# Optimization experiments

Hardware: AMD Instinct MI355X
Metric: run time of the kernel (lower is better)

Reference implementation:

```python
import jax, jax.numpy as jnp
import numpy as np

N_NODES = 30000
N_EDGES = 240000
N_GRAPHS = 300
IN_CH = 5


def _bn(x, p):
    # inference batchnorm; p = stack([gamma, beta, running_mean, running_var]), shape (4, C)
    g, b, m, v = p
    return g * (x - m) * jax.lax.rsqrt(v + 1e-5) + b


def _gatv2(x, src, dst, wl, bl, wr, br, att, bias, heads, outc, concat):
    # PyG GATv2Conv: e_ij = att . leaky_relu(lin_l(x_j) + lin_r(x_i)), softmax over edges into i,
    # out_i = sum_j alpha_ij * lin_l(x_j)
    n = x.shape[0]
    xl = (x @ wl + bl).reshape(n, heads, outc)  # source-side transform
    xr = (x @ wr + br).reshape(n, heads, outc)  # target-side transform
    e = jax.nn.leaky_relu(xl[src] + xr[dst], 0.2)          # [E, H, C]
    logit = jnp.einsum('ehc,hc->eh', e, att)               # [E, H]
    lmax = jax.ops.segment_max(logit, dst, num_segments=n)
    lmax = jnp.where(jnp.isfinite(lmax), lmax, 0.0)        # empty segments -> 0
    ex = jnp.exp(logit - lmax[dst])
    den = jax.ops.segment_sum(ex, dst, num_segments=n)
    alpha = ex / (den[dst] + 1e-16)                        # PyG softmax eps
    out = jax.ops.segment_sum(xl[src] * alpha[..., None], dst, num_segments=n)
    out = out.reshape(n, heads * outc) if concat else out.mean(axis=1)
    return out + bias


def _forward(x, edge_index, batch, w_in, b_in, bn_in,
             g1_wl, g1_bl, g1_wr, g1_br, g1_att, g1_bias, bn1,
             g2_wl, g2_bl, g2_wr, g2_br, g2_att, g2_bias, bn2,
             g3_wl, g3_bl, g3_wr, g3_br, g3_att, g3_bias, bn3,
             c_w1, c_b1, c_bn, c_w2, c_b2, c_w3, c_b3):
    n = x.shape[0]
    loops = jnp.arange(n)
    src = jnp.concatenate([edge_index[0], loops])  # add_self_loops=True
    dst = jnp.concatenate([edge_index[1], loops])
    h = jax.nn.relu(_bn(x @ w_in + b_in, bn_in))
    h = jax.nn.elu(_bn(_gatv2(h, src, dst, g1_wl, g1_bl, g1_wr, g1_br, g1_att, g1_bias, 4, 64, True), bn1))
    h = jax.nn.elu(_bn(_gatv2(h, src, dst, g2_wl, g2_bl, g2_wr, g2_br, g2_att, g2_bias, 4, 64, True), bn2))
    h = jax.nn.elu(_bn(_gatv2(h, src, dst, g3_wl, g3_bl, g3_wr, g3_br, g3_att, g3_bias, 1, 128, False), bn3))
    cnt = jax.ops.segment_sum(jnp.ones((n,), h.dtype), batch, num_segments=N_GRAPHS)
    mean = jax.ops.segment_sum(h, batch, num_segments=N_GRAPHS) / jnp.maximum(cnt, 1.0)[:, None]
    mx = jax.ops.segment_max(h, batch, num_segments=N_GRAPHS)
    mx = jnp.where(jnp.isfinite(mx), mx, 0.0)
    g = jnp.concatenate([mean, mx], axis=1)                # (B, 256)
    z = jax.nn.relu(_bn(g @ c_w1 + c_b1, c_bn))
    z = jax.nn.relu(z @ c_w2 + c_b2)
    return jax.nn.log_softmax(z @ c_w3 + c_b3, axis=-1)    # (B, 2)


def setup_inputs() -> dict:
    base = jax.random.key(0)
    k = lambda i: jax.random.fold_in(base, i)
    def lin(i, fi, fo):
        return jax.random.normal(k(i), (fi, fo), jnp.float32) / np.sqrt(np.float32(fi))
    def vec(i, c):
        return jax.random.normal(k(i), (c,), jnp.float32) * 0.05
    def bn(i, c):
        g = jax.random.uniform(k(i), (c,), jnp.float32) + 0.5
        b = jax.random.normal(jax.random.fold_in(k(i), 1), (c,), jnp.float32) * 0.1
        return jnp.stack([g, b, jnp.zeros((c,), jnp.float32), jnp.ones((c,), jnp.float32)])
    def att(i, h, c):
        return jax.random.normal(k(i), (h, c), jnp.float32) / np.sqrt(np.float32(c))
    return dict(
        x=jax.random.normal(k(0), (N_NODES, IN_CH), jnp.float32),
        edge_index=jax.random.randint(k(1), (2, N_EDGES), 0, N_NODES),
        batch=jnp.sort(jax.random.randint(k(2), (N_NODES,), 0, N_GRAPHS)),
        w_in=lin(3, IN_CH, 64), b_in=vec(4, 64), bn_in=bn(5, 64),
        g1_wl=lin(6, 64, 256), g1_bl=vec(7, 256), g1_wr=lin(8, 64, 256), g1_br=vec(9, 256),
        g1_att=att(10, 4, 64), g1_bias=vec(11, 256), bn1=bn(12, 256),
        g2_wl=lin(13, 256, 256), g2_bl=vec(14, 256), g2_wr=lin(15, 256, 256), g2_br=vec(16, 256),
        g2_att=att(17, 4, 64), g2_bias=vec(18, 256), bn2=bn(19, 256),
        g3_wl=lin(20, 256, 128), g3_bl=vec(21, 128), g3_wr=lin(22, 256, 128), g3_br=vec(23, 128),
        g3_att=att(24, 1, 128), g3_bias=vec(25, 128), bn3=bn(26, 128),
        c_w1=lin(27, 256, 128), c_b1=vec(28, 128), c_bn=bn(29, 128),
        c_w2=lin(30, 128, 64), c_b2=vec(31, 64),
        c_w3=lin(32, 64, 2), c_b3=vec(33, 2),
    )


def reference(x, edge_index, batch, w_in, b_in, bn_in,
              g1_wl, g1_bl, g1_wr, g1_br, g1_att, g1_bias, bn1,
              g2_wl, g2_bl, g2_wr, g2_br, g2_att, g2_bias, bn2,
              g3_wl, g3_bl, g3_wr, g3_br, g3_att, g3_bias, bn3,
              c_w1, c_b1, c_bn, c_w2, c_b2, c_w3, c_b3):
    return _forward(x, edge_index, batch, w_in, b_in, bn_in,
                    g1_wl, g1_bl, g1_wr, g1_br, g1_att, g1_bias, bn1,
                    g2_wl, g2_bl, g2_wr, g2_br, g2_att, g2_bias, bn2,
                    g3_wl, g3_bl, g3_wr, g3_br, g3_att, g3_bias, bn3,
                    c_w1, c_b1, c_bn, c_w2, c_b2, c_w3, c_b3)
```

## Files before the change

### kernel.cpp

```cpp
#include <hip/hip_runtime.h>
#include <math.h>

#define N_NODES  30000
#define N_EDGES  240000
#define E_TOT    270000
#define N_GRAPHS 300
#define NCH      118

typedef _Float16 half8 __attribute__((ext_vector_type(8)));
typedef _Float16 half4 __attribute__((ext_vector_type(4)));
typedef _Float16 half2v __attribute__((ext_vector_type(2)));
typedef float float4v __attribute__((ext_vector_type(4)));

static inline int cdiv(int a, int b) { return (a + b - 1) / b; }

__device__ inline void wp_dev(const float* __restrict__ W, _Float16* __restrict__ Wt,
                              int K, int CO, int gtid, int T) {
    int tot = K * CO;
    for (int i = gtid; i < tot; i += T) {
        int k = i / CO, c = i - k * CO;
        Wt[(size_t)c * K + k] = (_Float16)W[i];
    }
}

__global__ void hist_wprep_input(const int* __restrict__ ei, int* __restrict__ deg,
                                 const float* __restrict__ x, const float* __restrict__ w_in,
                                 const float* __restrict__ b_in, const float* __restrict__ bn_in,
                                 _Float16* __restrict__ a16,
                                 const float* __restrict__ w1l, const float* __restrict__ w1r,
                                 const float* __restrict__ w2l, const float* __restrict__ w2r,
                                 const float* __restrict__ w3l, const float* __restrict__ w3r,
                                 _Float16* __restrict__ t1l, _Float16* __restrict__ t1r,
                                 _Float16* __restrict__ t2l, _Float16* __restrict__ t2r,
                                 _Float16* __restrict__ t3l, _Float16* __restrict__ t3r) {
    int gtid = blockIdx.x * blockDim.x + threadIdx.x;
    int T = gridDim.x * blockDim.x;
    for (int e = gtid; e < E_TOT; e += T) {
        int d = (e < N_EDGES) ? ei[N_EDGES + e] : e - N_EDGES;
        atomicAdd(&deg[d], 1);
    }
    wp_dev(w1l, t1l, 64, 256, gtid, T);
    wp_dev(w1r, t1r, 64, 256, gtid, T);
    wp_dev(w2l, t2l, 256, 256, gtid, T);
    wp_dev(w2r, t2r, 256, 256, gtid, T);
    wp_dev(w3l, t3l, 256, 128, gtid, T);
    wp_dev(w3r, t3r, 256, 128, gtid, T);

    int lane = threadIdx.x & 63;
    int wv = blockIdx.x * (blockDim.x >> 6) + (threadIdx.x >> 6);
    int NW = gridDim.x * (blockDim.x >> 6);
    float g = bn_in[lane], be = bn_in[64 + lane];
    float m = bn_in[128 + lane], va = bn_in[192 + lane];
    float rs = rsqrtf(va + 1e-5f);
    float wcol[5];
#pragma unroll
    for (int ci = 0; ci < 5; ++ci) wcol[ci] = w_in[ci * 64 + lane];
    float bb = b_in[lane];
    for (int n = wv; n < N_NODES; n += NW) {
        float xv = (lane < 5) ? x[n * 5 + lane] : 0.f;
        float acc = bb;
#pragma unroll
        for (int ci = 0; ci < 5; ++ci)
            acc = fmaf(__shfl(xv, ci, 64), wcol[ci], acc);
        acc = g * (acc - m) * rs + be;
        a16[(size_t)n * 64 + lane] = (_Float16)fmaxf(acc, 0.f);
    }
}

__global__ __launch_bounds__(256)
void scan_all(const int* __restrict__ deg, const int* __restrict__ batch,
              int* __restrict__ row_start, int* __restrict__ gstart) {
    __shared__ int red[256];
    __shared__ int s[256];
    const int b = blockIdx.x, t = threadIdx.x;
    int pre = 0;
    for (int i = t; i < b * 256; i += 256) pre += deg[i];
    red[t] = pre;
    __syncthreads();
    for (int off = 128; off; off >>= 1) {
        if (t < off) red[t] += red[t + off];
        __syncthreads();
    }
    int base = red[0];
    int gid = b * 256 + t;
    int v = (gid < N_NODES) ? deg[gid] : 0;
    s[t] = v;
    __syncthreads();
    for (int off = 1; off < 256; off <<= 1) {
        int u = (t >= off) ? s[t - off] : 0;
        __syncthreads();
        s[t] += u;
        __syncthreads();
    }
    if (gid < N_NODES) row_start[gid] = base + s[t] - v;
    if (b == 0 && t == 0) row_start[N_NODES] = E_TOT;
    if (b == 0) {
        for (int g = t; g <= N_GRAPHS; g += 256) {
            int lo = 0, hi = N_NODES;
            while (lo < hi) {
                int mid = (lo + hi) >> 1;
                if (batch[mid] < g) lo = mid + 1;
                else                hi = mid;
            }
            gstart[g] = lo;
        }
    }
}

template<int K, int COUT, int SCAT>
__global__ __launch_bounds__(256, 3)
void gemm_mfma(const _Float16* __restrict__ A,
               const _Float16* __restrict__ Wtl, const float* __restrict__ bl,
               const _Float16* __restrict__ Wtr, const float* __restrict__ br,
               _Float16* __restrict__ outl, _Float16* __restrict__ outr,
               const int* __restrict__ ei, const int* __restrict__ row_start,
               int* __restrict__ cnt, int* __restrict__ esrc, int N) {
    constexpr int BM = 128, BN = 128, BK = 64;
    constexpr int LDK = BK + 8;
    constexpr int CSL = COUT / BN > 0 ? COUT / BN : 1;
    if (SCAT && blockIdx.y == 2 * CSL) {
        int gtid = blockIdx.x * blockDim.x + threadIdx.x;
        int T = gridDim.x * blockDim.x;
        for (int e = gtid; e < E_TOT; e += T) {
            int s, d;
            if (e < N_EDGES) { s = ei[e]; d = ei[N_EDGES + e]; }
            else             { s = e - N_EDGES; d = s; }
            int slot = row_start[d] + atomicAdd(&cnt[d], 1);
            esrc[slot] = s;
        }
        return;
    }
    __shared__ _Float16 As[BM][LDK];
    __shared__ _Float16 Bs[BN][LDK];
    const int tid  = threadIdx.x;
    const int wave = tid >> 6;
    const int lane = tid & 63;
    const int l15  = lane & 15;
    const int lq   = lane >> 4;
    const int n0   = blockIdx.x * BM;
    const int sel  = blockIdx.y / CSL;
    const int col0 = (blockIdx.y % CSL) * BN;
    const _Float16* Wt = sel ? Wtr : Wtl;
    const float* bias  = sel ? br : bl;
    _Float16* out      = sel ? outr : outl;

    float4v acc[2][8];
#pragma unroll
    for (int mi = 0; mi < 2; ++mi)
#pragma unroll
        for (int nt = 0; nt < 8; ++nt)
#pragma unroll
            for (int r = 0; r < 4; ++r) acc[mi][nt][r] = 0.f;

    for (int kt = 0; kt < K; kt += BK) {
#pragma unroll
        for (int p = 0; p < 4; ++p) {
            int idx = p * 256 + tid;
            int row = idx >> 3;
            int ch  = (idx & 7) * 8;
            int gn  = n0 + row;
            half8 v = {};
            if (gn < N) v = *(const half8*)(A + (size_t)gn * K + kt + ch);
            *(half8*)(&As[row][ch]) = v;
        }
#pragma unroll
        for (int p = 0; p < 4; ++p) {
            int idx = p * 256 + tid;
            int row = idx >> 3;
            int ch  = (idx & 7) * 8;
            half8 v = *(const half8*)(Wt + (size_t)(col0 + row) * K + kt + ch);
            *(half8*)(&Bs[row][ch]) = v;
        }
        __syncthreads();
#pragma unroll
        for (int kk = 0; kk < BK; kk += 32) {
            half8 af0 = *(const half8*)(&As[wave * 32 + l15][kk + lq * 8]);
            half8 af1 = *(const half8*)(&As[wave * 32 + 16 + l15][kk + lq * 8]);
#pragma unroll
            for (int nt = 0; nt < 8; ++nt) {
                half8 bf = *(const half8*)(&Bs[nt * 16 + l15][kk + lq * 8]);
                acc[0][nt] = __builtin_amdgcn_mfma_f32_16x16x32_f16(af0, bf, acc[0][nt], 0, 0, 0);
                acc[1][nt] = __builtin_amdgcn_mfma_f32_16x16x32_f16(af1, bf, acc[1][nt], 0, 0, 0);
            }
        }
        __syncthreads();
    }
#pragma unroll
    for (int mi = 0; mi < 2; ++mi)
#pragma unroll
        for (int nt = 0; nt < 8; ++nt) {
            int col = col0 + nt * 16 + l15;
            float bv = bias[col];
#pragma unroll
            for (int r = 0; r < 4; ++r) {
                int row = n0 + wave * 32 + mi * 16 + lq * 4 + r;
                if (row < N)
                    out[(size_t)row * COUT + col] = (_Float16)(acc[mi][nt][r] + bv);
            }
        }
}

template<typename TOUT>
__global__ __launch_bounds__(256)
void gat_gather4(const _Float16* __restrict__ xl, const _Float16* __restrict__ xr,
                 const int* __restrict__ row_start, const int* __restrict__ esrc,
                 const float* __restrict__ att, const float* __restrict__ gbias,
                 const float* __restrict__ bnp, TOUT* __restrict__ out) {
    constexpr int HC = 256, PER = 4, GROUP = 16;
    int node = (blockIdx.x * blockDim.x + threadIdx.x) >> 6;
    int lane = threadIdx.x & 63;
    if (node >= N_NODES) return;
    const int base = lane * PER;

    float rr[PER], av[PER], acc[PER];
    {
        half4 rv = *(const half4*)(xr + (size_t)node * HC + base);
#pragma unroll
        for (int k = 0; k < PER; ++k) rr[k] = (float)rv[k];
        *(float4*)av = *(const float4*)(att + base);
    }
#pragma unroll
    for (int k = 0; k < PER; ++k) acc[k] = 0.f;

    float l = 0.f;
    const int j0 = row_start[node], j1 = row_start[node + 1];
    for (int jc = j0; jc < j1; jc += 64) {
        int nedge = min(64, j1 - jc);
        int ev = (jc + lane < j1) ? esrc[jc + lane] : 0;
        for (int jj = 0; jj < nedge; jj += 4) {
            int s[4];
            bool val[4];
#pragma unroll
            for (int u = 0; u < 4; ++u) {
                int idx = jj + u;
                val[u] = idx < nedge;
                s[u] = __shfl(ev, val[u] ? idx : jj, 64);
            }
            float xs[4][PER];
#pragma unroll
            for (int u = 0; u < 4; ++u) {
                half4 xv = *(const half4*)(xl + (size_t)s[u] * HC + base);
#pragma unroll
                for (int k = 0; k < PER; ++k) xs[u][k] = (float)xv[k];
            }
            float pz[4];
#pragma unroll
            for (int u = 0; u < 4; ++u) {
                float pp = 0.f;
#pragma unroll
                for (int k = 0; k < PER; ++k) {
                    float v = xs[u][k] + rr[k];
                    v = (v > 0.f) ? v : 0.2f * v;
                    pp = fmaf(v, av[k], pp);
                }
                pz[u] = pp;
            }
#pragma unroll
            for (int off = GROUP / 2; off; off >>= 1) {
#pragma unroll
                for (int u = 0; u < 4; ++u) pz[u] += __shfl_xor(pz[u], off, 64);
            }
            float w[4];
#pragma unroll
            for (int u = 0; u < 4; ++u) w[u] = val[u] ? __expf(pz[u]) : 0.f;
            l += (w[0] + w[1]) + (w[2] + w[3]);
#pragma unroll
            for (int k = 0; k < PER; ++k)
                acc[k] += fmaf(w[0], xs[0][k],
                          fmaf(w[1], xs[1][k],
                          fmaf(w[2], xs[2][k], w[3] * xs[3][k])));
        }
    }
    float inv = 1.f / (l + 1e-16f);
    float o[PER];
#pragma unroll
    for (int k = 0; k < PER; ++k) {
        float v = fmaf(acc[k], inv, gbias[base + k]);
        float g  = bnp[base + k], be = bnp[HC + base + k];
        float mm = bnp[2 * HC + base + k], va = bnp[3 * HC + base + k];
        v = g * (v - mm) * rsqrtf(va + 1e-5f) + be;
        o[k] = (v > 0.f) ? v : (__expf(v) - 1.f);
    }
    half4 ov;
#pragma unroll
    for (int k = 0; k < PER; ++k) ov[k] = (_Float16)o[k];
    *(half4*)((_Float16*)out + (size_t)node * HC + base) = ov;
}

__global__ __launch_bounds__(256)
void gat_gather1(const _Float16* __restrict__ xl, const _Float16* __restrict__ xr,
                 const int* __restrict__ row_start, const int* __restrict__ esrc,
                 const float* __restrict__ att, const float* __restrict__ gbias,
                 const float* __restrict__ bnp, float* __restrict__ out) {
    constexpr int HC = 128, PER = 4;
    int node = (blockIdx.x * blockDim.x + threadIdx.x) >> 6;
    int lane = threadIdx.x & 63;
    if (node >= N_NODES) return;
    const int half = lane >> 5;
    const int base = (lane & 31) * PER;

    float rr[PER], av[PER], acc[PER];
    {
        half4 rv = *(const half4*)(xr + (size_t)node * HC + base);
#pragma unroll
        for (int k = 0; k < PER; ++k) rr[k] = (float)rv[k];
        *(float4*)av = *(const float4*)(att + base);
    }
#pragma unroll
    for (int k = 0; k < PER; ++k) acc[k] = 0.f;

    float l = 0.f;
    const int j0 = row_start[node], j1 = row_start[node + 1];
    for (int jc = j0; jc < j1; jc += 64) {
        int nedge = min(64, j1 - jc);
        int ev = (jc + lane < j1) ? esrc[jc + lane] : 0;
        for (int jj = 0; jj < nedge; jj += 8) {
            int s[4];
            bool val[4];
#pragma unroll
            for (int u = 0; u < 4; ++u) {
                int idx = jj + 2 * u + half;
                val[u] = idx < nedge;
                s[u] = __shfl(ev, val[u] ? idx : jj, 64);
            }
            float xs[4][PER];
#pragma unroll
            for (int u = 0; u < 4; ++u) {
                half4 xv = *(const half4*)(xl + (size_t)s[u] * HC + base);
#pragma unroll
                for (int k = 0; k < PER; ++k) xs[u][k] = (float)xv[k];
            }
            float pz[4];
#pragma unroll
            for (int u = 0; u < 4; ++u) {
                float pp = 0.f;
#pragma unroll
                for (int k = 0; k < PER; ++k) {
                    float v = xs[u][k] + rr[k];
                    v = (v > 0.f) ? v : 0.2f * v;
                    pp = fmaf(v, av[k], pp);
                }
                pz[u] = pp;
            }
#pragma unroll
            for (int off = 16; off; off >>= 1) {
#pragma unroll
                for (int u = 0; u < 4; ++u) pz[u] += __shfl_xor(pz[u], off, 64);
            }
            float w[4];
#pragma unroll
            for (int u = 0; u < 4; ++u) w[u] = val[u] ? __expf(pz[u]) : 0.f;
            l += (w[0] + w[1]) + (w[2] + w[3]);
#pragma unroll
            for (int k = 0; k < PER; ++k)
                acc[k] += fmaf(w[0], xs[0][k],
                          fmaf(w[1], xs[1][k],
                          fmaf(w[2], xs[2][k], w[3] * xs[3][k])));
        }
    }
    l += __shfl_xor(l, 32, 64);
#pragma unroll
    for (int k = 0; k < PER; ++k) acc[k] += __shfl_xor(acc[k], 32, 64);

    if (half == 0) {
        float inv = 1.f / (l + 1e-16f);
        float o[PER];
#pragma unroll
        for (int k = 0; k < PER; ++k) {
            float v = fmaf(acc[k], inv, gbias[base + k]);
            float g  = bnp[base + k], be = bnp[HC + base + k];
            float mm = bnp[2 * HC + base + k], va = bnp[3 * HC + base + k];
            v = g * (v - mm) * rsqrtf(va + 1e-5f) + be;
            o[k] = (v > 0.f) ? v : (__expf(v) - 1.f);
        }
        *(float4*)(out + (size_t)node * HC + base) = *(float4*)o;
    }
}

__global__ void pool_cls(const float* __restrict__ h, const int* __restrict__ gstart,
                         const float* __restrict__ w1, const float* __restrict__ b1,
                         const float* __restrict__ bnp,
                         const float* __restrict__ w2, const float* __restrict__ b2,
                         const float* __restrict__ w3, const float* __restrict__ b3,
                         float* __restrict__ out) {
    __shared__ float sg[256];
    __shared__ float sz1[128];
    __shared__ float sz2[64];
    __shared__ float sz3[2];
    int g = blockIdx.x, t = threadIdx.x;
    int a = gstart[g], b = gstart[g + 1];
    float sum = 0.f, mx = -INFINITY;
    for (int i = a; i < b; ++i) {
        float v = h[(size_t)i * 128 + t];
        sum += v;
        mx = fmaxf(mx, v);
    }
    sg[t]       = sum / fmaxf((float)(b - a), 1.f);
    sg[128 + t] = (b > a) ? mx : 0.f;
    __syncthreads();
    float acc = b1[t];
    for (int i = 0; i < 256; ++i) acc += sg[i] * w1[i * 128 + t];
    float ga = bnp[t], be = bnp[128 + t], m = bnp[256 + t], va = bnp[384 + t];
    acc = ga * (acc - m) * rsqrtf(va + 1e-5f) + be;
    sz1[t] = fmaxf(acc, 0.f);
    __syncthreads();
    if (t < 64) {
        float a2 = b2[t];
        for (int i = 0; i < 128; ++i) a2 += sz1[i] * w2[i * 64 + t];
        sz2[t] = fmaxf(a2, 0.f);
    }
    __syncthreads();
    if (t < 2) {
        float a3 = b3[t];
        for (int i = 0; i < 64; ++i) a3 += sz2[i] * w3[i * 2 + t];
        sz3[t] = a3;
    }
    __syncthreads();
    if (t < 2) {
        float mm = fmaxf(sz3[0], sz3[1]);
        float lse = mm + logf(expf(sz3[0] - mm) + expf(sz3[1] - mm));
        out[g * 2 + t] = sz3[t] - lse;
    }
}

extern "C" void kernel_launch(void* const* d_in, const int* in_sizes, int n_in,
                              void* d_out, int out_size, void* d_ws, size_t ws_size,
                              hipStream_t stream) {
    const float* x       = (const float*)d_in[0];
    const int*   ei      = (const int*)d_in[1];
    const int*   batch   = (const int*)d_in[2];
    const float* w_in    = (const float*)d_in[3];
    const float* b_in    = (const float*)d_in[4];
    const float* bn_in   = (const float*)d_in[5];
    const float* g1_wl   = (const float*)d_in[6];
    const float* g1_bl   = (const float*)d_in[7];
    const float* g1_wr   = (const float*)d_in[8];
    const float* g1_br   = (const float*)d_in[9];
    const float* g1_att  = (const float*)d_in[10];
    const float* g1_bias = (const float*)d_in[11];
    const float* bn1     = (const float*)d_in[12];
    const float* g2_wl   = (const float*)d_in[13];
    const float* g2_bl   = (const float*)d_in[14];
    const float* g2_wr   = (const float*)d_in[15];
    const float* g2_br   = (const float*)d_in[16];
    const float* g2_att  = (const float*)d_in[17];
    const float* g2_bias = (const float*)d_in[18];
    const float* bn2     = (const float*)d_in[19];
    const float* g3_wl   = (const float*)d_in[20];
    const float* g3_bl   = (const float*)d_in[21];
    const float* g3_wr   = (const float*)d_in[22];
    const float* g3_br   = (const float*)d_in[23];
    const float* g3_att  = (const float*)d_in[24];
    const float* g3_bias = (const float*)d_in[25];
    const float* bn3     = (const float*)d_in[26];
    const float* c_w1    = (const float*)d_in[27];
    const float* c_b1    = (const float*)d_in[28];
    const float* c_bn    = (const float*)d_in[29];
    const float* c_w2    = (const float*)d_in[30];
    const float* c_b2    = (const float*)d_in[31];
    const float* c_w3    = (const float*)d_in[32];
    const float* c_b3    = (const float*)d_in[33];
    float* out = (float*)d_out;

    const size_t NHC = (size_t)N_NODES * 256;
    _Float16* a16  = (_Float16*)d_ws;
    _Float16* xl16 = a16 + NHC;
    _Float16* xr16 = xl16 + NHC;
    _Float16* wt = xr16 + NHC;
    _Float16* wt1l = wt;            _Float16* wt1r = wt + 16384;
    _Float16* wt2l = wt + 32768;    _Float16* wt2r = wt + 98304;
    _Float16* wt3l = wt + 163840;   _Float16* wt3r = wt + 196608;
    float* fbase = (float*)(wt + 262144);
    float* bufD = fbase;
    int* iw = (int*)(bufD + (size_t)N_NODES * 128);
    int* deg       = iw;            int* cnt    = iw + 30000;
    int* row_start = iw + 90128;
    int* esrc      = iw + 120129;
    int* gstart    = iw + 390429;

    const int BT = 256;
    const int NT128 = cdiv(N_NODES, 128);

    hipMemsetAsync(deg, 0, 60000 * sizeof(int), stream);

    hist_wprep_input<<<1024, BT, 0, stream>>>(ei, deg, x, w_in, b_in, bn_in, a16,
                                              g1_wl, g1_wr, g2_wl, g2_wr, g3_wl, g3_wr,
                                              wt1l, wt1r, wt2l, wt2r, wt3l, wt3r);
    scan_all<<<NCH, 256, 0, stream>>>(deg, batch, row_start, gstart);

    gemm_mfma<64, 256, 1><<<dim3(NT128, 5), 256, 0, stream>>>(
        a16, wt1l, g1_bl, wt1r, g1_br, xl16, xr16, ei, row_start, cnt, esrc, N_NODES);
    gat_gather4<_Float16><<<cdiv(N_NODES * 64, BT), BT, 0, stream>>>(
        xl16, xr16, row_start, esrc, g1_att, g1_bias, bn1, a16);

    gemm_mfma<256, 256, 0><<<dim3(NT128, 4), 256, 0, stream>>>(
        a16, wt2l, g2_bl, wt2r, g2_br, xl16, xr16, nullptr, nullptr, nullptr, nullptr, N_NODES);
    gat_gather4<_Float16><<<cdiv(N_NODES * 64, BT), BT, 0, stream>>>(
        xl16, xr16, row_start, esrc, g2_att, g2_bias, bn2, a16);

    gemm_mfma<256, 128, 0><<<dim3(NT128, 2), 256, 0, stream>>>(
        a16, wt3l, g3_bl, wt3r, g3_br, xl16, xr16, nullptr, nullptr, nullptr, nullptr, N_NODES);
    gat_gather1<<<cdiv(N_NODES * 64, BT), BT, 0, stream>>>(
        xl16, xr16, row_start, esrc, g3_att, g3_bias, bn3, bufD);

    pool_cls<<<N_GRAPHS, 128, 0, stream>>>(bufD, gstart, c_w1, c_b1, c_bn,
                                           c_w2, c_b2, c_w3, c_b3, out);
}
```

Baseline: 370.6 us.

## Split wave into four edge groups in 4-head GATv2 gather

The 4-head gather kernel now has each quarter-wave (16 lanes) handle one edge at a time, with 16 channels per lane loaded as two half8 vectors. Before, all 64 lanes covered one edge's 256 channels at 4 per lane and unrolled four edges. Partial softmax sums and accumulators are reduced across the four groups with xor-shuffles at the end, and only one group writes the output. This gives wider vector loads and a shorter per-edge head reduction, but costs more registers per lane and a final cross-group reduction.

```diff
diff --git a/kernel.cpp b/kernel.cpp
--- a/kernel.cpp
+++ b/kernel.cpp
@@ -200,24 +200,28 @@
         }
 }
 
-template<typename TOUT>
 __global__ __launch_bounds__(256)
 void gat_gather4(const _Float16* __restrict__ xl, const _Float16* __restrict__ xr,
                  const int* __restrict__ row_start, const int* __restrict__ esrc,
                  const float* __restrict__ att, const float* __restrict__ gbias,
-                 const float* __restrict__ bnp, TOUT* __restrict__ out) {
-    constexpr int HC = 256, PER = 4, GROUP = 16;
+                 const float* __restrict__ bnp, _Float16* __restrict__ out) {
+    constexpr int HC = 256, PER = 16;
     int node = (blockIdx.x * blockDim.x + threadIdx.x) >> 6;
     int lane = threadIdx.x & 63;
     if (node >= N_NODES) return;
-    const int base = lane * PER;
+    const int q    = lane >> 4;
+    const int base = (lane & 15) * PER;
 
     float rr[PER], av[PER], acc[PER];
     {
-        half4 rv = *(const half4*)(xr + (size_t)node * HC + base);
-#pragma unroll
-        for (int k = 0; k < PER; ++k) rr[k] = (float)rv[k];
-        *(float4*)av = *(const float4*)(att + base);
+        half8 r0 = *(const half8*)(xr + (size_t)node * HC + base);
+        half8 r1 = *(const half8*)(xr + (size_t)node * HC + base + 8);
+#pragma unroll
+        for (int k = 0; k < 8; ++k) { rr[k] = (float)r0[k]; rr[8 + k] = (float)r1[k]; }
+        *(float4*)(av)      = *(const float4*)(att + base);
+        *(float4*)(av + 4)  = *(const float4*)(att + base + 4);
+        *(float4*)(av + 8)  = *(const float4*)(att + base + 8);
+        *(float4*)(av + 12) = *(const float4*)(att + base + 12);
     }
 #pragma unroll
     for (int k = 0; k < PER; ++k) acc[k] = 0.f;
@@ -228,63 +232,53 @@
         int nedge = min(64, j1 - jc);
         int ev = (jc + lane < j1) ? esrc[jc + lane] : 0;
         for (int jj = 0; jj < nedge; jj += 4) {
-            int s[4];
-            bool val[4];
-#pragma unroll
-            for (int u = 0; u < 4; ++u) {
-                int idx = jj + u;
-                val[u] = idx < nedge;
-                s[u] = __shfl(ev, val[u] ? idx : jj, 64);
-            }
-            float xs[4][PER];
-#pragma unroll
-            for (int u = 0; u < 4; ++u) {
-                half4 xv = *(const half4*)(xl + (size_t)s[u] * HC + base);
-#pragma unroll
-                for (int k = 0; k < PER; ++k) xs[u][k] = (float)xv[k];
-            }
-            float pz[4];
-#pragma unroll
-            for (int u = 0; u < 4; ++u) {
-                float pp = 0.f;
-#pragma unroll
-                for (int k = 0; k < PER; ++k) {
-                    float v = xs[u][k] + rr[k];
-                    v = (v > 0.f) ? v : 0.2f * v;
-                    pp = fmaf(v, av[k], pp);
-                }
-                pz[u] = pp;
-            }
-#pragma unroll
-            for (int off = GROUP / 2; off; off >>= 1) {
-#pragma unroll
-                for (int u = 0; u < 4; ++u) pz[u] += __shfl_xor(pz[u], off, 64);
-            }
-            float w[4];
-#pragma unroll
-            for (int u = 0; u < 4; ++u) w[u] = val[u] ? __expf(pz[u]) : 0.f;
-            l += (w[0] + w[1]) + (w[2] + w[3]);
-#pragma unroll
-            for (int k = 0; k < PER; ++k)
-                acc[k] += fmaf(w[0], xs[0][k],
-                          fmaf(w[1], xs[1][k],
-                          fmaf(w[2], xs[2][k], w[3] * xs[3][k])));
-        }
-    }
-    float inv = 1.f / (l + 1e-16f);
-    float o[PER];
+            int idx = jj + q;
+            bool val = idx < nedge;
+            int s = __shfl(ev, val ? idx : jj, 64);
+            float xs[PER];
+            {
+                half8 x0 = *(const half8*)(xl + (size_t)s * HC + base);
+                half8 x1 = *(const half8*)(xl + (size_t)s * HC + base + 8);
+#pragma unroll
+                for (int k = 0; k < 8; ++k) { xs[k] = (float)x0[k]; xs[8 + k] = (float)x1[k]; }
+            }
+            float pp = 0.f;
+#pragma unroll
+            for (int k = 0; k < PER; ++k) {
+                float v = xs[k] + rr[k];
+                v = (v > 0.f) ? v : 0.2f * v;
+                pp = fmaf(v, av[k], pp);
+            }
+            pp += __shfl_xor(pp, 1, 64);
+            pp += __shfl_xor(pp, 2, 64);
+            float w = val ? __expf(pp) : 0.f;
+            l += w;
+#pragma unroll
+            for (int k = 0; k < PER; ++k) acc[k] = fmaf(w, xs[k], acc[k]);
+        }
+    }
+    l += __shfl_xor(l, 16, 64);
+    l += __shfl_xor(l, 32, 64);
 #pragma unroll
     for (int k = 0; k < PER; ++k) {
-        float v = fmaf(acc[k], inv, gbias[base + k]);
-        float g  = bnp[base + k], be = bnp[HC + base + k];
-        float mm = bnp[2 * HC + base + k], va = bnp[3 * HC + base + k];
-        v = g * (v - mm) * rsqrtf(va + 1e-5f) + be;
-        o[k] = (v > 0.f) ? v : (__expf(v) - 1.f);
-    }
-    half4 ov;
-#pragma unroll
-    for (int k = 0; k < PER; ++k) ov[k] = (_Float16)o[k];
-    *(half4*)((_Float16*)out + (size_t)node * HC + base) = ov;
+        acc[k] += __shfl_xor(acc[k], 16, 64);
+        acc[k] += __shfl_xor(acc[k], 32, 64);
+    }
+    if (q == 0) {
+        float inv = 1.f / (l + 1e-16f);
+        half8 o0, o1;
+#pragma unroll
+        for (int k = 0; k < PER; ++k) {
+            float v = fmaf(acc[k], inv, gbias[base + k]);
+            float g  = bnp[base + k], be = bnp[HC + base + k];
+            float mm = bnp[2 * HC + base + k], va = bnp[3 * HC + base + k];
+            v = g * (v - mm) * rsqrtf(va + 1e-5f) + be;
+            v = (v > 0.f) ? v : (__expf(v) - 1.f);
+            if (k < 8) o0[k] = (_Float16)v; else o1[k - 8] = (_Float16)v;
+        }
+        *(half8*)(out + (size_t)node * HC + base)     = o0;
+        *(half8*)(out + (size_t)node * HC + base + 8) = o1;
+    }
 }
 
 __global__ __launch_bounds__(256)
@@ -490,12 +484,12 @@
 
     gemm_mfma<64, 256, 1><<<dim3(NT128, 5), 256, 0, stream>>>(
         a16, wt1l, g1_bl, wt1r, g1_br, xl16, xr16, ei, row_start, cnt, esrc, N_NODES);
-    gat_gather4<_Float16><<<cdiv(N_NODES * 64, BT), BT, 0, stream>>>(
+    gat_gather4<<<cdiv(N_NODES * 64, BT), BT, 0, stream>>>(
         xl16, xr16, row_start, esrc, g1_att, g1_bias, bn1, a16);
 
     gemm_mfma<256, 256, 0><<<dim3(NT128, 4), 256, 0, stream>>>(
         a16, wt2l, g2_bl, wt2r, g2_br, xl16, xr16, nullptr, nullptr, nullptr, nullptr, N_NODES);
-    gat_gather4<_Float16><<<cdiv(N_NODES * 64, BT), BT, 0, stream>>>(
+    gat_gather4<<<cdiv(N_NODES * 64, BT), BT, 0, stream>>>(
         xl16, xr16, row_start, esrc, g2_att, g2_bias, bn2, a16);
 
     gemm_mfma<256, 128, 0><<<dim3(NT128, 2), 256, 0, stream>>>(
```

After: 405.8 us. 9.5% more time.
